# Kernel tuning notes

Hardware: AMD Instinct MI355X
Metric: run time of the kernel (lower is better)

Reference implementation:

```python
import jax, jax.numpy as jnp
import numpy as np

B, L, D, H = 4, 2048, 1024, 16
HD = D // H
SCALE = 1.0 / (D / H) ** 0.5


def setup_inputs() -> dict:
    key = jax.random.key(0)
    ks = jax.random.split(key, 11)
    s = 1.0 / np.sqrt(D)
    return {
        "q": jax.random.normal(ks[0], (B, L, D), jnp.float32),
        "k": jax.random.normal(ks[1], (B, L, D), jnp.float32),
        "v": jax.random.normal(ks[2], (B, L, D), jnp.float32),
        "Wq": jax.random.normal(ks[3], (D, D), jnp.float32) * s,
        "bq": jnp.zeros((D,), jnp.float32),
        "Wk": jax.random.normal(ks[4], (D, D), jnp.float32) * s,
        "bk": jnp.zeros((D,), jnp.float32),
        "Wv": jax.random.normal(ks[5], (D, D), jnp.float32) * s,
        "bv": jnp.zeros((D,), jnp.float32),
        "Wo": jax.random.normal(ks[6], (D, D), jnp.float32) * s,
        "bo": jnp.zeros((D,), jnp.float32),
    }


def _split_heads(x):
    # [b, l, h*d] -> [b, h, l, d]
    b, l, _ = x.shape
    return x.reshape(b, l, H, HD).transpose(0, 2, 1, 3)


def reference(q, k, v, Wq, bq, Wk, bk, Wv, bv, Wo, bo):
    # Linear projections (torch Linear: x @ W.T + b)
    qh = _split_heads(q @ Wq.T + bq)            # [b, h, l, d]
    kh = _split_heads(k @ Wk.T + bk)            # [b, h, l, d]
    vh = _split_heads(v @ Wv.T + bv)            # [b, h, l, d]
    scores = jnp.einsum('bhqd,bhkd->bhqk', qh, kh) * SCALE
    attn = jax.nn.softmax(scores, axis=-1)       # dropout p=0 -> identity
    out = jnp.einsum('bhqk,bhkd->bhqd', attn, vh)
    out = out.transpose(0, 2, 1, 3).reshape(q.shape[0], q.shape[1], D)
    return out @ Wo.T + bo
```

## Files before the change

kernel.cpp:

```cpp
#include <hip/hip_runtime.h>


#define Bsz 4
#define Lq 2048
#define Dm 1024
#define NH 16
#define HD 64
#define QSCALE 0.18033688011112042f

typedef unsigned short u16;
typedef __attribute__((ext_vector_type(4))) short bf16x4;
typedef __attribute__((ext_vector_type(8))) short short8;
typedef __attribute__((ext_vector_type(4))) float f32x4;

__device__ __forceinline__ f32x4 mfma16(bf16x4 a, bf16x4 b, f32x4 c) {
#if defined(__HIP_DEVICE_COMPILE__)
  return __builtin_amdgcn_mfma_f32_16x16x16bf16_1k(a, b, c, 0, 0, 0);
#else
  return c;
#endif
}
#define MFMA32(a, b, c) __builtin_amdgcn_mfma_f32_16x16x32_bf16(a, b, c, 0, 0, 0)

typedef __attribute__((address_space(3))) unsigned su32;
typedef __attribute__((address_space(1))) unsigned gu32;
__device__ __forceinline__ void gl_lds16(const u16* g, u16* l) {
  __builtin_amdgcn_global_load_lds((gu32*)(g), (su32*)(l), 16, 0, 0);
}

__device__ __forceinline__ u16 f2b(float x) {
  unsigned u = __builtin_bit_cast(unsigned, x);
  return (u16)((u + 0x7fffu + ((u >> 16) & 1u)) >> 16);
}
__device__ __forceinline__ unsigned pk2(float a, float b) {
  return (unsigned)f2b(a) | ((unsigned)f2b(b) << 16);
}
__device__ __forceinline__ bf16x4 pack4(float a, float b, float c, float d) {
  unsigned lo = __builtin_amdgcn_perm(__builtin_bit_cast(unsigned, b) + 0x8000u,
                                      __builtin_bit_cast(unsigned, a) + 0x8000u, 0x07060302u);
  unsigned hi = __builtin_amdgcn_perm(__builtin_bit_cast(unsigned, d) + 0x8000u,
                                      __builtin_bit_cast(unsigned, c) + 0x8000u, 0x07060302u);
  uint2 u; u.x = lo; u.y = hi;
  return __builtin_bit_cast(bf16x4, u);
}
__device__ __forceinline__ float fexp2(float x) {
#if __has_builtin(__builtin_amdgcn_exp2f)
  return __builtin_amdgcn_exp2f(x);
#else
  return exp2f(x);
#endif
}

__global__ void castk(const float* __restrict__ src, u16* __restrict__ dst, int n, float scale) {
  int i = (blockIdx.x * 256 + threadIdx.x) * 8;
  if (i >= n) return;
  float4 a = *(const float4*)(src + i);
  float4 b = *(const float4*)(src + i + 4);
  short8 o;
  o[0] = (short)f2b(a.x * scale); o[1] = (short)f2b(a.y * scale);
  o[2] = (short)f2b(a.z * scale); o[3] = (short)f2b(a.w * scale);
  o[4] = (short)f2b(b.x * scale); o[5] = (short)f2b(b.y * scale);
  o[6] = (short)f2b(b.z * scale); o[7] = (short)f2b(b.w * scale);
  *(short8*)(dst + i) = o;
}

__global__ void castw(const float* __restrict__ s0, const float* __restrict__ s1,
                      const float* __restrict__ s2, const float* __restrict__ s3,
                      u16* __restrict__ d0, u16* __restrict__ d1,
                      u16* __restrict__ d2, u16* __restrict__ d3) {
  const float* s; u16* d; float sc = 1.0f;
  switch (blockIdx.y) {
    case 0: s = s0; d = d0; sc = QSCALE; break;
    case 1: s = s1; d = d1; break;
    case 2: s = s2; d = d2; break;
    default: s = s3; d = d3; break;
  }
  int i = (blockIdx.x * 256 + threadIdx.x) * 8;
  float4 a = *(const float4*)(s + i);
  float4 b = *(const float4*)(s + i + 4);
  short8 o;
  o[0] = (short)f2b(a.x * sc); o[1] = (short)f2b(a.y * sc);
  o[2] = (short)f2b(a.z * sc); o[3] = (short)f2b(a.w * sc);
  o[4] = (short)f2b(b.x * sc); o[5] = (short)f2b(b.y * sc);
  o[6] = (short)f2b(b.z * sc); o[7] = (short)f2b(b.w * sc);
  *(short8*)(d + i) = o;
}

template<int MODE>
__global__ __launch_bounds__(256) void gemm2(
    const u16* __restrict__ A, const u16* __restrict__ Bt,
    const float* __restrict__ bias, void* __restrict__ C,
    int M, int N, int K, float bscale)
{
  __shared__ __align__(16) u16 As[128 * 32];
  __shared__ __align__(16) u16 Bs[128 * 32];
  const int tid  = threadIdx.x;
  const int lane = tid & 63;
  const int wave = tid >> 6;
  const int quad = lane >> 4;
  const int r16  = lane & 15;
  const int wm   = (wave >> 1) * 64;
  const int wn   = (wave & 1) * 64;
  const int m0   = blockIdx.y * 128;
  const int n0   = blockIdx.x * 128;

  const u16* ga = A  + (size_t)(m0 + wave * 32 + (lane >> 2)) * K + (lane & 3) * 8;
  const u16* gb = Bt + (size_t)(n0 + wave * 32 + (lane >> 2)) * K + (lane & 3) * 8;
  u16* la = As + wave * 1024;
  u16* lb = Bs + wave * 1024;

  f32x4 acc[4][4] = {};

  for (int k0 = 0; k0 < K; k0 += 32) {
    gl_lds16(ga + k0, la);
    gl_lds16(ga + k0 + (size_t)16 * K, la + 512);
    gl_lds16(gb + k0, lb);
    gl_lds16(gb + k0 + (size_t)16 * K, lb + 512);
    __syncthreads();

    short8 af[4], bfr[4];
#pragma unroll
    for (int mt = 0; mt < 4; ++mt) af[mt]  = *(const short8*)&As[(wm + mt * 16 + r16) * 32 + quad * 8];
#pragma unroll
    for (int nt = 0; nt < 4; ++nt) bfr[nt] = *(const short8*)&Bs[(wn + nt * 16 + r16) * 32 + quad * 8];
#pragma unroll
    for (int mt = 0; mt < 4; ++mt)
#pragma unroll
      for (int nt = 0; nt < 4; ++nt)
        acc[mt][nt] = MFMA32(af[mt], bfr[nt], acc[mt][nt]);
    __syncthreads();
  }

#pragma unroll
  for (int mt = 0; mt < 4; ++mt) {
#pragma unroll
    for (int nt = 0; nt < 4; ++nt) {
      int n = n0 + wn + nt * 16 + r16;
      float bv = bias ? bias[n] * bscale : 0.f;
      if (MODE == 2) {
        int m_base = m0 + wm + mt * 16 + quad * 4;
        int b = m_base >> 11, l0 = m_base & 2047;
        int h = n >> 6, d = n & 63;
        u16* dst = (u16*)C + (((size_t)(b * NH + h)) * HD + d) * Lq + l0;
        uint2 pkd;
        pkd.x = pk2(acc[mt][nt][0] + bv, acc[mt][nt][1] + bv);
        pkd.y = pk2(acc[mt][nt][2] + bv, acc[mt][nt][3] + bv);
        *(uint2*)dst = pkd;
      } else {
#pragma unroll
        for (int j = 0; j < 4; ++j) {
          int m = m0 + wm + mt * 16 + quad * 4 + j;
          float v = acc[mt][nt][j] + bv;
          if (MODE == 1) {
            int b = m >> 11, l = m & 2047;
            int h = n >> 6,  d = n & 63;
            ((u16*)C)[(((size_t)(b * NH + h)) * Lq + l) * HD + d] = f2b(v);
          } else {
            ((float*)C)[(size_t)m * N + n] = v;
          }
        }
      }
    }
  }
}

__global__ __launch_bounds__(256) void attn3(
    const u16* __restrict__ Qh, const u16* __restrict__ Kh,
    const u16* __restrict__ Vtg, u16* __restrict__ Oa)
{
  const int bh = blockIdx.y;
  const int qt = blockIdx.x;
  const int tid = threadIdx.x, lane = tid & 63, wave = tid >> 6;
  const int quad = lane >> 4, r16 = lane & 15;

  __shared__ __align__(16) u16 Ks[64][72];
  __shared__ __align__(16) u16 Vt[64][72];

  const int qbase = qt * 128 + wave * 32;
  short8 aq[2][2];
#pragma unroll
  for (int qf = 0; qf < 2; ++qf) {
    const size_t qrow = ((size_t)bh * Lq + qbase + qf * 16 + r16) * HD;
    aq[qf][0] = *(const short8*)(Qh + qrow + quad * 8);
    aq[qf][1] = *(const short8*)(Qh + qrow + 32 + quad * 8);
  }

  f32x4 oacc[2][4] = {};
  float lsum[2] = {0.f, 0.f};

  const int srow = tid >> 2;
  const int scid = (tid & 3) * 16;
  const u16* kg = Kh  + ((size_t)bh * Lq + srow) * HD + scid;
  const u16* vg = Vtg + ((size_t)bh * HD + srow) * Lq + scid;

  short8 pk0 = *(const short8*)(kg);
  short8 pk1 = *(const short8*)(kg + 8);
  short8 pv0 = *(const short8*)(vg);
  short8 pv1 = *(const short8*)(vg + 8);

  for (int t = 0; t < 32; ++t) {
    __syncthreads();
    *(short8*)&Ks[srow][scid]     = pk0;
    *(short8*)&Ks[srow][scid + 8] = pk1;
    *(short8*)&Vt[srow][scid]     = pv0;
    *(short8*)&Vt[srow][scid + 8] = pv1;
    __syncthreads();
    if (t < 31) {
      const u16* kgn = kg + (size_t)(t + 1) * 64 * HD;
      const u16* vgn = vg + (t + 1) * 64;
      pk0 = *(const short8*)(kgn);
      pk1 = *(const short8*)(kgn + 8);
      pv0 = *(const short8*)(vgn);
      pv1 = *(const short8*)(vgn + 8);
    }

#pragma unroll
    for (int mt = 0; mt < 4; ++mt) {
      short8 kf0 = *(const short8*)&Ks[mt * 16 + r16][quad * 8];
      short8 kf1 = *(const short8*)&Ks[mt * 16 + r16][32 + quad * 8];
      bf16x4 vf[4];
#pragma unroll
      for (int nt = 0; nt < 4; ++nt)
        vf[nt] = *(const bf16x4*)&Vt[nt * 16 + r16][mt * 16 + quad * 4];
#pragma unroll
      for (int qf = 0; qf < 2; ++qf) {
        f32x4 z = {};
        z = MFMA32(kf0, aq[qf][0], z);
        z = MFMA32(kf1, aq[qf][1], z);
        float p0 = fexp2(z[0]);
        float p1 = fexp2(z[1]);
        float p2 = fexp2(z[2]);
        float p3 = fexp2(z[3]);
        lsum[qf] += (p0 + p1) + (p2 + p3);
        bf16x4 pb = pack4(p0, p1, p2, p3);
#pragma unroll
        for (int nt = 0; nt < 4; ++nt)
          oacc[qf][nt] = mfma16(vf[nt], pb, oacc[qf][nt]);
      }
    }
  }

  const int b = bh >> 4, h = bh & 15;
  float linv[2];
#pragma unroll
  for (int qf = 0; qf < 2; ++qf) {
    float r = lsum[qf];
    r += __shfl_xor(r, 16);
    r += __shfl_xor(r, 32);
    linv[qf] = 1.0f / r;
  }
#pragma unroll
  for (int qf = 0; qf < 2; ++qf) {
    int q = qbase + qf * 16 + r16;
    size_t rowb = ((size_t)(b * Lq + q)) * Dm + h * HD;
#pragma unroll
    for (int nt = 0; nt < 4; ++nt) {
      f32x4 o = oacc[qf][nt];
      uint2 pkd;
      pkd.x = pk2(o[0] * linv[qf], o[1] * linv[qf]);
      pkd.y = pk2(o[2] * linv[qf], o[3] * linv[qf]);
      *(uint2*)&Oa[rowb + nt * 16 + quad * 4] = pkd;
    }
  }
}

extern "C" void kernel_launch(void* const* d_in, const int* in_sizes, int n_in,
                              void* d_out, int out_size, void* d_ws, size_t ws_size,
                              hipStream_t stream) {
  const float* q  = (const float*)d_in[0];
  const float* k  = (const float*)d_in[1];
  const float* v  = (const float*)d_in[2];
  const float* Wq = (const float*)d_in[3];
  const float* bq = (const float*)d_in[4];
  const float* Wk = (const float*)d_in[5];
  const float* bk = (const float*)d_in[6];
  const float* Wv = (const float*)d_in[7];
  const float* bv = (const float*)d_in[8];
  const float* Wo = (const float*)d_in[9];
  const float* bo = (const float*)d_in[10];

  u16* abuf = (u16*)d_ws;
  u16* Qh   = abuf + 8388608;
  u16* Kh   = Qh   + 8388608;
  u16* Vtg  = Kh   + 8388608;
  u16* wqb  = Vtg  + 8388608;
  u16* wkb  = wqb  + 1048576;
  u16* wvb  = wkb  + 1048576;
  u16* wob  = wvb  + 1048576;

  castw<<<dim3(512, 4), 256, 0, stream>>>(Wq, Wk, Wv, Wo, wqb, wkb, wvb, wob);

  dim3 gp(Dm / 128, (Bsz * Lq) / 128);
  const int NA = Bsz * Lq * Dm;

  castk<<<NA / 2048, 256, 0, stream>>>(q, abuf, NA, 1.0f);
  gemm2<1><<<gp, 256, 0, stream>>>(abuf, wqb, bq, Qh, Bsz * Lq, Dm, Dm, QSCALE);
  castk<<<NA / 2048, 256, 0, stream>>>(k, abuf, NA, 1.0f);
  gemm2<1><<<gp, 256, 0, stream>>>(abuf, wkb, bk, Kh, Bsz * Lq, Dm, Dm, 1.0f);
  castk<<<NA / 2048, 256, 0, stream>>>(v, abuf, NA, 1.0f);
  gemm2<2><<<gp, 256, 0, stream>>>(abuf, wvb, bv, Vtg, Bsz * Lq, Dm, Dm, 1.0f);

  attn3<<<dim3(Lq / 128, Bsz * NH), 256, 0, stream>>>(Qh, Kh, Vtg, abuf);

  gemm2<3><<<gp, 256, 0, stream>>>(abuf, wob, bo, (float*)d_out, Bsz * Lq, Dm, Dm, 1.0f);
}
```

Before: 410.5 us.

## Batch QKV casts and projections into single launches, retile output projection

The three input casts become one kernel with a z-grid over q/k/v, and the three projection GEMMs become one launch of 1536 blocks instead of three of 512. This removes launch gaps and tail effects between the serial small launches, at the cost of a workspace that now holds three bf16 activation copies. The output projection uses a 128x64 tile so it launches 1024 blocks, which gives more parallelism across CUs but reuses each loaded A tile over fewer columns.

Result: faster. 371.6 us (-9.5%).

```diff
diff --git a/kernel.cpp b/kernel.cpp
--- a/kernel.cpp
+++ b/kernel.cpp
@@ -51,17 +51,19 @@
 #endif
 }
 
-__global__ void castk(const float* __restrict__ src, u16* __restrict__ dst, int n, float scale) {
+__global__ void castk3(const float* __restrict__ q, const float* __restrict__ k,
+                       const float* __restrict__ v, u16* __restrict__ dst) {
+  const float* s = blockIdx.y == 0 ? q : (blockIdx.y == 1 ? k : v);
+  u16* d = dst + (size_t)blockIdx.y * (Bsz * Lq * Dm);
   int i = (blockIdx.x * 256 + threadIdx.x) * 8;
-  if (i >= n) return;
-  float4 a = *(const float4*)(src + i);
-  float4 b = *(const float4*)(src + i + 4);
+  float4 a = *(const float4*)(s + i);
+  float4 b = *(const float4*)(s + i + 4);
   short8 o;
-  o[0] = (short)f2b(a.x * scale); o[1] = (short)f2b(a.y * scale);
-  o[2] = (short)f2b(a.z * scale); o[3] = (short)f2b(a.w * scale);
-  o[4] = (short)f2b(b.x * scale); o[5] = (short)f2b(b.y * scale);
-  o[6] = (short)f2b(b.z * scale); o[7] = (short)f2b(b.w * scale);
-  *(short8*)(dst + i) = o;
+  o[0] = (short)f2b(a.x); o[1] = (short)f2b(a.y);
+  o[2] = (short)f2b(a.z); o[3] = (short)f2b(a.w);
+  o[4] = (short)f2b(b.x); o[5] = (short)f2b(b.y);
+  o[6] = (short)f2b(b.z); o[7] = (short)f2b(b.w);
+  *(short8*)(d + i) = o;
 }
 
 __global__ void castw(const float* __restrict__ s0, const float* __restrict__ s1,
@@ -86,14 +88,20 @@
   *(short8*)(d + i) = o;
 }
 
-template<int MODE>
-__global__ __launch_bounds__(256) void gemm2(
-    const u16* __restrict__ A, const u16* __restrict__ Bt,
-    const float* __restrict__ bias, void* __restrict__ C,
-    int M, int N, int K, float bscale)
+__global__ __launch_bounds__(256) void qkv_gemm(
+    const u16* __restrict__ Ab,
+    const u16* __restrict__ Wqb, const u16* __restrict__ Wkb, const u16* __restrict__ Wvb,
+    const float* __restrict__ bq, const float* __restrict__ bk, const float* __restrict__ bv,
+    u16* __restrict__ Qh, u16* __restrict__ Kh, u16* __restrict__ Vtg)
 {
   __shared__ __align__(16) u16 As[128 * 32];
   __shared__ __align__(16) u16 Bs[128 * 32];
+  const int z = blockIdx.z;
+  const u16* A  = Ab + (size_t)z * (Bsz * Lq * Dm);
+  const u16* Bt = z == 0 ? Wqb : (z == 1 ? Wkb : Wvb);
+  const float* bias = z == 0 ? bq : (z == 1 ? bk : bv);
+  const float bscale = z == 0 ? QSCALE : 1.0f;
+
   const int tid  = threadIdx.x;
   const int lane = tid & 63;
   const int wave = tid >> 6;
@@ -104,18 +112,18 @@
   const int m0   = blockIdx.y * 128;
   const int n0   = blockIdx.x * 128;
 
-  const u16* ga = A  + (size_t)(m0 + wave * 32 + (lane >> 2)) * K + (lane & 3) * 8;
-  const u16* gb = Bt + (size_t)(n0 + wave * 32 + (lane >> 2)) * K + (lane & 3) * 8;
+  const u16* ga = A  + (size_t)(m0 + wave * 32 + (lane >> 2)) * Dm + (lane & 3) * 8;
+  const u16* gb = Bt + (size_t)(n0 + wave * 32 + (lane >> 2)) * Dm + (lane & 3) * 8;
   u16* la = As + wave * 1024;
   u16* lb = Bs + wave * 1024;
 
   f32x4 acc[4][4] = {};
 
-  for (int k0 = 0; k0 < K; k0 += 32) {
+  for (int k0 = 0; k0 < Dm; k0 += 32) {
     gl_lds16(ga + k0, la);
-    gl_lds16(ga + k0 + (size_t)16 * K, la + 512);
+    gl_lds16(ga + k0 + 16 * Dm, la + 512);
     gl_lds16(gb + k0, lb);
-    gl_lds16(gb + k0 + (size_t)16 * K, lb + 512);
+    gl_lds16(gb + k0 + 16 * Dm, lb + 512);
     __syncthreads();
 
     short8 af[4], bfr[4];
@@ -136,29 +144,81 @@
 #pragma unroll
     for (int nt = 0; nt < 4; ++nt) {
       int n = n0 + wn + nt * 16 + r16;
-      float bv = bias ? bias[n] * bscale : 0.f;
-      if (MODE == 2) {
+      float bv_ = bias[n] * bscale;
+      if (z == 2) {
         int m_base = m0 + wm + mt * 16 + quad * 4;
         int b = m_base >> 11, l0 = m_base & 2047;
         int h = n >> 6, d = n & 63;
-        u16* dst = (u16*)C + (((size_t)(b * NH + h)) * HD + d) * Lq + l0;
+        u16* dst = Vtg + (((size_t)(b * NH + h)) * HD + d) * Lq + l0;
         uint2 pkd;
-        pkd.x = pk2(acc[mt][nt][0] + bv, acc[mt][nt][1] + bv);
-        pkd.y = pk2(acc[mt][nt][2] + bv, acc[mt][nt][3] + bv);
+        pkd.x = pk2(acc[mt][nt][0] + bv_, acc[mt][nt][1] + bv_);
+        pkd.y = pk2(acc[mt][nt][2] + bv_, acc[mt][nt][3] + bv_);
         *(uint2*)dst = pkd;
       } else {
+        u16* dst = z == 0 ? Qh : Kh;
 #pragma unroll
         for (int j = 0; j < 4; ++j) {
           int m = m0 + wm + mt * 16 + quad * 4 + j;
-          float v = acc[mt][nt][j] + bv;
-          if (MODE == 1) {
-            int b = m >> 11, l = m & 2047;
-            int h = n >> 6,  d = n & 63;
-            ((u16*)C)[(((size_t)(b * NH + h)) * Lq + l) * HD + d] = f2b(v);
-          } else {
-            ((float*)C)[(size_t)m * N + n] = v;
-          }
+          int b = m >> 11, l = m & 2047;
+          int h = n >> 6,  d = n & 63;
+          dst[(((size_t)(b * NH + h)) * Lq + l) * HD + d] = f2b(acc[mt][nt][j] + bv_);
         }
+      }
+    }
+  }
+}
+
+__global__ __launch_bounds__(256) void gemm_wo(
+    const u16* __restrict__ A, const u16* __restrict__ Bt,
+    const float* __restrict__ bias, float* __restrict__ C)
+{
+  __shared__ __align__(16) u16 As[128 * 32];
+  __shared__ __align__(16) u16 Bs[64 * 32];
+  const int tid  = threadIdx.x;
+  const int lane = tid & 63;
+  const int wave = tid >> 6;
+  const int quad = lane >> 4;
+  const int r16  = lane & 15;
+  const int wm   = wave * 32;
+  const int m0   = blockIdx.y * 128;
+  const int n0   = blockIdx.x * 64;
+
+  const u16* ga = A  + (size_t)(m0 + wave * 32 + (lane >> 2)) * Dm + (lane & 3) * 8;
+  const u16* gb = Bt + (size_t)(n0 + wave * 16 + (lane >> 2)) * Dm + (lane & 3) * 8;
+  u16* la = As + wave * 1024;
+  u16* lb = Bs + wave * 512;
+
+  f32x4 acc[2][4] = {};
+
+  for (int k0 = 0; k0 < Dm; k0 += 32) {
+    gl_lds16(ga + k0, la);
+    gl_lds16(ga + k0 + 16 * Dm, la + 512);
+    gl_lds16(gb + k0, lb);
+    __syncthreads();
+
+    short8 af[2], bfr[4];
+#pragma unroll
+    for (int mt = 0; mt < 2; ++mt) af[mt]  = *(const short8*)&As[(wm + mt * 16 + r16) * 32 + quad * 8];
+#pragma unroll
+    for (int nt = 0; nt < 4; ++nt) bfr[nt] = *(const short8*)&Bs[(nt * 16 + r16) * 32 + quad * 8];
+#pragma unroll
+    for (int mt = 0; mt < 2; ++mt)
+#pragma unroll
+      for (int nt = 0; nt < 4; ++nt)
+        acc[mt][nt] = MFMA32(af[mt], bfr[nt], acc[mt][nt]);
+    __syncthreads();
+  }
+
+#pragma unroll
+  for (int mt = 0; mt < 2; ++mt) {
+#pragma unroll
+    for (int nt = 0; nt < 4; ++nt) {
+      int n = n0 + nt * 16 + r16;
+      float bv = bias[n];
+#pragma unroll
+      for (int j = 0; j < 4; ++j) {
+        int m = m0 + wm + mt * 16 + quad * 4 + j;
+        C[(size_t)m * Dm + n] = acc[mt][nt][j] + bv;
       }
     }
   }
@@ -279,28 +339,22 @@
   const float* Wo = (const float*)d_in[9];
   const float* bo = (const float*)d_in[10];
 
+  const int NA = Bsz * Lq * Dm;
   u16* abuf = (u16*)d_ws;
-  u16* Qh   = abuf + 8388608;
-  u16* Kh   = Qh   + 8388608;
-  u16* Vtg  = Kh   + 8388608;
-  u16* wqb  = Vtg  + 8388608;
+  u16* Qh   = abuf + (size_t)3 * NA;
+  u16* Kh   = Qh   + NA;
+  u16* Vtg  = Kh   + NA;
+  u16* wqb  = Vtg  + NA;
   u16* wkb  = wqb  + 1048576;
   u16* wvb  = wkb  + 1048576;
   u16* wob  = wvb  + 1048576;
 
   castw<<<dim3(512, 4), 256, 0, stream>>>(Wq, Wk, Wv, Wo, wqb, wkb, wvb, wob);
-
-  dim3 gp(Dm / 128, (Bsz * Lq) / 128);
-  const int NA = Bsz * Lq * Dm;
-
-  castk<<<NA / 2048, 256, 0, stream>>>(q, abuf, NA, 1.0f);
-  gemm2<1><<<gp, 256, 0, stream>>>(abuf, wqb, bq, Qh, Bsz * Lq, Dm, Dm, QSCALE);
-  castk<<<NA / 2048, 256, 0, stream>>>(k, abuf, NA, 1.0f);
-  gemm2<1><<<gp, 256, 0, stream>>>(abuf, wkb, bk, Kh, Bsz * Lq, Dm, Dm, 1.0f);
-  castk<<<NA / 2048, 256, 0, stream>>>(v, abuf, NA, 1.0f);
-  gemm2<2><<<gp, 256, 0, stream>>>(abuf, wvb, bv, Vtg, Bsz * Lq, Dm, Dm, 1.0f);
+  castk3<<<dim3(NA / 2048, 3), 256, 0, stream>>>(q, k, v, abuf);
+
+  qkv_gemm<<<dim3(8, 64, 3), 256, 0, stream>>>(abuf, wqb, wkb, wvb, bq, bk, bv, Qh, Kh, Vtg);
 
   attn3<<<dim3(Lq / 128, Bsz * NH), 256, 0, stream>>>(Qh, Kh, Vtg, abuf);
 
-  gemm2<3><<<gp, 256, 0, stream>>>(abuf, wob, bo, (float*)d_out, Bsz * Lq, Dm, Dm, 1.0f);
-}
+  gemm_wo<<<dim3(16, 64), 256, 0, stream>>>(abuf, wob, bo, (float*)d_out);
+}
```
